# Performance work log

Measured on AMD Instinct MI355X. Metric: run time of the kernel, lower is better.

The kernel has to match this reference:

```python
import jax, jax.numpy as jnp
import numpy as np

BN_EPS = 1e-5

def conv3x3(x, w, b):
    # x: (B,C,H,W), w: (O,C,3,3) -> (B,O,H,W), padding=1 == SAME for 3x3 stride 1
    y = jax.lax.conv_general_dilated(x, w, window_strides=(1, 1), padding='SAME',
                                     dimension_numbers=('NCHW', 'OIHW', 'NCHW'))
    return y + b[None, :, None, None]

def batchnorm(x, gamma, beta):
    # training-mode BatchNorm2d: per-channel batch stats over (N,H,W), biased variance
    mean = jnp.mean(x, axis=(0, 2, 3), keepdims=True)
    var = jnp.var(x, axis=(0, 2, 3), keepdims=True)
    return (x - mean) * jax.lax.rsqrt(var + BN_EPS) * gamma[None, :, None, None] + beta[None, :, None, None]


def setup_inputs() -> dict:
    key = jax.random.key(0)
    ks = jax.random.split(key, 4)
    B, E, T, Fr, H = 16, 16, 1024, 80, 8
    # xavier-ish scale for conv weights
    w_in = jax.random.normal(ks[1], (3 * H, E, 3, 3), jnp.float32) * (1.0 / np.sqrt(E * 9))
    w_out = jax.random.normal(ks[2], (E, 2 * H, 3, 3), jnp.float32) * (1.0 / np.sqrt(2 * H * 9))
    return {
        'x': jax.random.normal(ks[0], (B, E, T, Fr), jnp.float32),
        'w_in': w_in,
        'b_in': jnp.zeros((3 * H,), jnp.float32),
        'w_out': w_out,
        'b_out': jnp.zeros((E,), jnp.float32),
        'gq': jnp.ones((H,), jnp.float32), 'bq': jnp.zeros((H,), jnp.float32),
        'gk': jnp.ones((H,), jnp.float32), 'bk': jnp.zeros((H,), jnp.float32),
        'gv': jnp.ones((H,), jnp.float32), 'bv': jnp.zeros((H,), jnp.float32),
        'go': jnp.ones((E,), jnp.float32), 'bo': jnp.zeros((E,), jnp.float32),
    }


def reference(x, w_in, b_in, w_out, b_out, gq, bq, gk, bk, gv, bv, go, bo):
    B, E, T, Fr = x.shape
    H = w_in.shape[0] // 3
    scaling = E ** (-0.5)  # head_dim == embed_dim in this module

    qkv = conv3x3(x, w_in, b_in)                      # (B, 3H, T, F)
    q, k, v = jnp.split(qkv, 3, axis=1)               # each (B, H, T, F)
    q = q * scaling

    q = jax.nn.relu(batchnorm(q, gq, bq)).reshape(B * H, T, Fr)
    k = jax.nn.relu(batchnorm(k, gk, bk)).reshape(B * H, T, Fr)
    v = jax.nn.relu(batchnorm(v, gv, bv)).reshape(B * H, T, Fr)

    # time-axis attention: (BH,T,F) x (BH,S,F) -> (BH,T,S)
    aw_t = jax.nn.softmax(jnp.einsum('btf,bsf->bts', q, k), axis=-1)
    attn_t = jnp.einsum('bts,bsf->btf', aw_t, v)      # (BH, T, F)

    # freq-axis attention: q^T @ k -> (BH,F,F); then @ v^T -> (BH,F,T)
    aw_f = jax.nn.softmax(jnp.einsum('btf,btg->bfg', q, k), axis=-1)
    attn_f = jnp.einsum('bfg,btg->bft', aw_f, v)      # (BH, F, T)

    attn_t = attn_t.reshape(B, H, T, Fr)
    attn_f = attn_f.transpose(0, 2, 1).reshape(B, H, T, Fr)
    attn = jnp.concatenate([attn_t, attn_f], axis=1)  # (B, 2H, T, F)

    out = jax.nn.relu(batchnorm(conv3x3(attn, w_out, b_out), go, bo))  # (B, E, T, F)
    aw_t_avg = aw_t.reshape(B, H, T, T).sum(axis=1) / H                # (B, T, T)
    return out, aw_t_avg
```

## Files before the change

kernel.cpp:

```cpp
#include <hip/hip_runtime.h>
#include <cstdint>
#include <cstddef>

#define NB 16
#define NT 1024
#define NF 80
#define NH 8
#define FP 96
#define FS 84
#define SP 1032
#define KP 108
#define VP 264

typedef _Float16 v8h __attribute__((ext_vector_type(8)));
typedef _Float16 v4h __attribute__((ext_vector_type(4)));
typedef _Float16 v2h __attribute__((ext_vector_type(2)));
typedef float v4f __attribute__((ext_vector_type(4)));

static const size_t OUT_ELEMS = (size_t)NB * 16 * NT * NF;

__global__ __launch_bounds__(256) void cl_k(const float* __restrict__ src,
                                            _Float16* __restrict__ dst) {
  const int b = blockIdx.y, t0 = blockIdx.x * 16;
  for (int i = threadIdx.x; i < 16 * FS; i += 256) {
    int lt = i / FS, s = i % FS;
    int t = t0 + lt, f = s - 1;
    v8h lo = (v8h)(_Float16)0.f, hi = (v8h)(_Float16)0.f;
    if (f >= 0 && f < NF) {
#pragma unroll
      for (int c = 0; c < 8; ++c)
        lo[c] = (_Float16)src[((size_t)(b * 16 + c) * NT + t) * NF + f];
#pragma unroll
      for (int c = 0; c < 8; ++c)
        hi[c] = (_Float16)src[((size_t)(b * 16 + 8 + c) * NT + t) * NF + f];
    }
    _Float16* d = dst + ((size_t)(b * NT + t) * FS + s) * 16;
    *(v8h*)d = lo;
    *(v8h*)(d + 8) = hi;
  }
}

template <int OCT, int OSTRIDE, bool QSCALE, bool PADOUT>
__global__ __launch_bounds__(512) void conv_mfma_k(
    const _Float16* __restrict__ xcl, const float* __restrict__ w,
    const float* __restrict__ bias, _Float16* __restrict__ out, int CO) {
  __shared__ _Float16 axt[18][FS * 16];
  __shared__ _Float16 wlds[3][2][OCT * 16][32];
  __shared__ float blds[32];
  const int b = blockIdx.y, t0 = blockIdx.x * 16;
  const int tid = threadIdx.x;
  const int NW = 3 * 2 * OCT * 16 * 32;
  for (int i = tid; i < NW; i += 512) {
    int kk = i % 32;
    int oc = (i / 32) % (OCT * 16);
    int ck = (i / (32 * OCT * 16)) % 2;
    int kt = i / (64 * OCT * 16);
    int kg = ck * 32 + kk;
    float v = 0.f;
    if (oc < CO && kg < 48) {
      int c = kg & 15, kf = kg >> 4;
      v = w[((oc * 16 + c) * 3 + kt) * 3 + kf];
      if (QSCALE && oc < 8) v *= 0.25f;
    }
    wlds[kt][ck][oc][kk] = (_Float16)v;
  }
  if (tid < 32) {
    float v = (tid < CO) ? bias[tid] : 0.f;
    if (QSCALE && tid < 8) v *= 0.25f;
    blds[tid] = v;
  }
  for (int i = tid; i < 18 * 168; i += 512) {
    int r = i / 168, j = i % 168;
    int t = t0 + r - 1;
    int4 v = {0, 0, 0, 0};
    if (t >= 0 && t < NT)
      v = ((const int4*)(xcl + (size_t)(b * NT + t) * FS * 16))[j];
    ((int4*)axt[r])[j] = v;
  }
  __syncthreads();
  const int wv = tid >> 6, l = tid & 63, lg = l >> 4, lm = l & 15;
  v8h bfr[3][2][OCT];
#pragma unroll
  for (int kt = 0; kt < 3; ++kt)
#pragma unroll
    for (int ck = 0; ck < 2; ++ck)
#pragma unroll
      for (int ot = 0; ot < OCT; ++ot)
        bfr[kt][ck][ot] = *(const v8h*)&wlds[kt][ck][ot * 16 + lm][lg * 8];
#pragma unroll
  for (int li = 0; li < 2; ++li) {
    const int lt = wv * 2 + li;
    const int tt = t0 + lt;
#pragma unroll
    for (int f0 = 0; f0 < 80; f0 += 16) {
      v4f acc[OCT];
#pragma unroll
      for (int ot = 0; ot < OCT; ++ot) acc[ot] = (v4f){0.f, 0.f, 0.f, 0.f};
#pragma unroll
      for (int kt = 0; kt < 3; ++kt)
#pragma unroll
        for (int ck = 0; ck < 2; ++ck) {
          v8h afr =
              *(const v8h*)&axt[lt + kt][(f0 + lm) * 16 + ck * 32 + lg * 8];
#pragma unroll
          for (int ot = 0; ot < OCT; ++ot)
            acc[ot] = __builtin_amdgcn_mfma_f32_16x16x32_f16(
                afr, bfr[kt][ck][ot], acc[ot], 0, 0, 0);
        }
#pragma unroll
      for (int ot = 0; ot < OCT; ++ot) {
        int oc = ot * 16 + lm;
        if (oc < CO) {
          float bv = blds[oc];
          v4h o;
#pragma unroll
          for (int r = 0; r < 4; ++r) o[r] = (_Float16)(acc[ot][r] + bv);
          *(v4h*)(out + ((size_t)(b * CO + oc) * NT + tt) * OSTRIDE + f0 +
                  lg * 4) = o;
        }
      }
    }
  }
  if constexpr (PADOUT) {
    for (int i = tid; i < CO * 16 * 2; i += 512) {
      int oc = i / 32, lt2 = (i / 2) % 16, half = i & 1;
      int4 z = {0, 0, 0, 0};
      ((int4*)(out + ((size_t)(b * CO + oc) * NT + t0 + lt2) * OSTRIDE +
               80))[half] = z;
    }
  }
}

__global__ __launch_bounds__(256) void bn_stats_h_k(
    const _Float16* __restrict__ x, float* __restrict__ partials) {
  const int b = blockIdx.x, c = blockIdx.y;
  const v8h* p = (const v8h*)(x + (size_t)(b * 24 + c) * NT * FP);
  float s = 0.f, s2 = 0.f;
  for (int i = threadIdx.x; i < NT * FP / 8; i += 256) {
    v8h v = p[i];
#pragma unroll
    for (int j = 0; j < 8; ++j) {
      float f = (float)v[j];
      s += f;
      s2 += f * f;
    }
  }
  __shared__ float rs[256], rs2[256];
  rs[threadIdx.x] = s;
  rs2[threadIdx.x] = s2;
  __syncthreads();
  for (int off = 128; off > 0; off >>= 1) {
    if ((int)threadIdx.x < off) {
      rs[threadIdx.x] += rs[threadIdx.x + off];
      rs2[threadIdx.x] += rs2[threadIdx.x + off];
    }
    __syncthreads();
  }
  if (threadIdx.x == 0) {
    partials[(c * 16 + b) * 2 + 0] = rs[0];
    partials[(c * 16 + b) * 2 + 1] = rs2[0];
  }
}

__global__ __launch_bounds__(256) void bn_stats_y_k(
    const _Float16* __restrict__ x, float* __restrict__ partials) {
  const int b = blockIdx.x, c = blockIdx.y;
  const v8h* p = (const v8h*)(x + (size_t)(b * 16 + c) * (NT * NF));
  float s = 0.f, s2 = 0.f;
  for (int i = threadIdx.x; i < NT * NF / 8; i += 256) {
    v8h v = p[i];
#pragma unroll
    for (int j = 0; j < 8; ++j) {
      float f = (float)v[j];
      s += f;
      s2 += f * f;
    }
  }
  __shared__ float rs[256], rs2[256];
  rs[threadIdx.x] = s;
  rs2[threadIdx.x] = s2;
  __syncthreads();
  for (int off = 128; off > 0; off >>= 1) {
    if ((int)threadIdx.x < off) {
      rs[threadIdx.x] += rs[threadIdx.x + off];
      rs2[threadIdx.x] += rs2[threadIdx.x + off];
    }
    __syncthreads();
  }
  if (threadIdx.x == 0) {
    partials[(c * 16 + b) * 2 + 0] = rs[0];
    partials[(c * 16 + b) * 2 + 1] = rs2[0];
  }
}

__global__ void bn_finalize_k(const float* __restrict__ partials,
                              float* __restrict__ stats, int C) {
  int c = threadIdx.x;
  if (c < C) {
    float s = 0.f, s2 = 0.f;
    for (int i = 0; i < 16; ++i) {
      s += partials[(c * 16 + i) * 2 + 0];
      s2 += partials[(c * 16 + i) * 2 + 1];
    }
    const float N = 16.0f * (float)(NT * NF);
    float mean = s / N;
    float var = s2 / N - mean * mean;
    stats[c * 2 + 0] = mean;
    stats[c * 2 + 1] = rsqrtf(var + 1e-5f);
  }
}

__global__ __launch_bounds__(256) void bn_apply_qkv_k(
    _Float16* __restrict__ qkv, const float* __restrict__ stats,
    const float* __restrict__ gq, const float* __restrict__ bq,
    const float* __restrict__ gk, const float* __restrict__ bk,
    const float* __restrict__ gv, const float* __restrict__ bv) {
  const size_t n8 = (size_t)NB * 24 * NT * 12;
  const size_t stride = (size_t)gridDim.x * blockDim.x;
  for (size_t idx = (size_t)blockIdx.x * blockDim.x + threadIdx.x; idx < n8;
       idx += stride) {
    int fc = (int)(idx % 12);
    if (fc >= 10) continue;
    int c = (int)((idx / (NT * 12)) % 24);
    float g, be;
    if (c < 8) { g = gq[c]; be = bq[c]; }
    else if (c < 16) { g = gk[c - 8]; be = bk[c - 8]; }
    else { g = gv[c - 16]; be = bv[c - 16]; }
    float mean = stats[c * 2 + 0], invstd = stats[c * 2 + 1];
    v8h v = ((v8h*)qkv)[idx];
#pragma unroll
    for (int j = 0; j < 8; ++j) {
      float f = (float)v[j];
      f = fmaxf((f - mean) * invstd * g + be, 0.f);
      v[j] = (_Float16)f;
    }
    ((v8h*)qkv)[idx] = v;
  }
}

__global__ __launch_bounds__(256) void vtrans_k(
    const _Float16* __restrict__ qkv, _Float16* __restrict__ vT) {
  __shared__ _Float16 tile[128 * 100];
  const int tc = blockIdx.x, bh = blockIdx.y;
  const int b = bh >> 3, h = bh & 7;
  const int t0 = tc * 128;
  const _Float16* src = qkv + ((size_t)(b * 24 + 16 + h) * NT + t0) * FP;
  const int tid = threadIdx.x;
  for (int i = tid; i < 1536; i += 256) {
    int row = i / 12, c = i % 12;
    int4 v = ((const int4*)src)[i];
    int2* d = (int2*)&tile[row * 100 + c * 8];
    d[0] = make_int2(v.x, v.y);
    d[1] = make_int2(v.z, v.w);
  }
  __syncthreads();
  _Float16* dst = vT + (size_t)bh * 80 * NT + t0;
  for (int i = tid; i < 1280; i += 256) {
    int f = i / 16, c8 = i % 16;
    v8h v;
#pragma unroll
    for (int j = 0; j < 8; ++j) v[j] = tile[(c8 * 8 + j) * 100 + f];
    *(v8h*)(dst + (size_t)f * NT + c8 * 8) = v;
  }
}

__global__ __launch_bounds__(512) void time_attn_k(
    const _Float16* __restrict__ qkv, const _Float16* __restrict__ vT,
    float* __restrict__ attn_out, float* __restrict__ aw_avg) {
  __shared__ _Float16 s_lds[32 * SP];
  __shared__ _Float16 q_lds[32 * KP];
  __shared__ _Float16 kst[256 * KP];
  __shared__ float inv_lds[32];
  const int b = blockIdx.y, t0 = blockIdx.x * 32;
  const int tid = threadIdx.x;
  const int w = tid >> 6, l = tid & 63, lg = l >> 4, lm = l & 15;
  const int grp = tid >> 5, lane = tid & 31;
  float avg[2][32];
#pragma unroll
  for (int rr = 0; rr < 2; ++rr)
#pragma unroll
    for (int k = 0; k < 32; ++k) avg[rr][k] = 0.f;

  int4 rb[6];
  auto gloadK = [&](const _Float16* base, int chunk) {
    const int4* src = (const int4*)(base + (size_t)chunk * 256 * FP);
#pragma unroll
    for (int u = 0; u < 6; ++u) rb[u] = src[tid + u * 512];
  };
  auto lwriteK = [&]() {
#pragma unroll
    for (int u = 0; u < 6; ++u) {
      int i = tid + u * 512, row = i / 12, j = i % 12;
      int2* d = (int2*)&kst[row * KP + j * 8];
      d[0] = make_int2(rb[u].x, rb[u].y);
      d[1] = make_int2(rb[u].z, rb[u].w);
    }
  };
  auto gloadV = [&](const int4* vt4, int chunk) {
#pragma unroll
    for (int u = 0; u < 5; ++u) {
      int i = tid + u * 512, row = i >> 5, c = i & 31;
      rb[u] = vt4[row * 128 + chunk * 32 + c];
    }
  };
  auto lwriteV = [&]() {
#pragma unroll
    for (int u = 0; u < 5; ++u) {
      int i = tid + u * 512, row = i >> 5, c = i & 31;
      *(int4*)&kst[row * VP + c * 8] = rb[u];
    }
  };

  gloadK(qkv + (size_t)(b * 24 + 8) * NT * FP, 0);

  for (int h = 0; h < NH; ++h) {
    const _Float16* qb = qkv + ((size_t)(b * 24 + h) * NT + t0) * FP;
    const _Float16* kb = qkv + (size_t)(b * 24 + 8 + h) * NT * FP;
    const int4* vt4 = (const int4*)(vT + (size_t)(b * 8 + h) * 80 * NT);
    int4 qreg = {0, 0, 0, 0};
    if (tid < 384) qreg = ((const int4*)qb)[tid];
    lwriteK();
    if (tid < 384) {
      int row = tid / 12, j = tid % 12;
      int2* d = (int2*)&q_lds[row * KP + j * 8];
      d[0] = make_int2(qreg.x, qreg.y);
      d[1] = make_int2(qreg.z, qreg.w);
    }
    gloadK(kb, 1);
    __syncthreads();
    v8h afr[2][3];
#pragma unroll
    for (int qt = 0; qt < 2; ++qt)
#pragma unroll
      for (int kk = 0; kk < 3; ++kk) {
        v4h a0 = *(const v4h*)&q_lds[(qt * 16 + lm) * KP + kk * 32 + lg * 8];
        v4h a1 =
            *(const v4h*)&q_lds[(qt * 16 + lm) * KP + kk * 32 + lg * 8 + 4];
        afr[qt][kk] = __builtin_shufflevector(a0, a1, 0, 1, 2, 3, 4, 5, 6, 7);
      }
    v4f accO[2][5];
#pragma unroll
    for (int qt = 0; qt < 2; ++qt)
#pragma unroll
      for (int ft = 0; ft < 5; ++ft) accO[qt][ft] = (v4f){0.f, 0.f, 0.f, 0.f};

    for (int s = 0; s < 8; ++s) {
      if (s == 4) {
#pragma unroll
        for (int rr = 0; rr < 2; ++rr) {
          const int row = grp + rr * 16;
          _Float16* srow = &s_lds[row * SP];
          float m = -1e30f;
#pragma unroll
          for (int k = 0; k < 16; ++k) {
            v2h e2 = *(const v2h*)&srow[lane * 2 + k * 64];
            m = fmaxf(m, fmaxf((float)e2[0], (float)e2[1]));
          }
#pragma unroll
          for (int mk = 16; mk; mk >>= 1) m = fmaxf(m, __shfl_xor(m, mk, 32));
          float d = 0.f;
#pragma unroll
          for (int k = 0; k < 16; ++k) {
            v2h e2 = *(const v2h*)&srow[lane * 2 + k * 64];
            float e0 = __expf((float)e2[0] - m);
            float e1 = __expf((float)e2[1] - m);
            d += e0 + e1;
            v2h w2;
            w2[0] = (_Float16)e0;
            w2[1] = (_Float16)e1;
            *(v2h*)&srow[lane * 2 + k * 64] = w2;
          }
#pragma unroll
          for (int mk = 16; mk; mk >>= 1) d += __shfl_xor(d, mk, 32);
          float inv = 1.f / d;
          if (lane == 0) inv_lds[row] = inv;
#pragma unroll
          for (int k = 0; k < 16; ++k) {
            v2h e2 = *(const v2h*)&srow[lane * 2 + k * 64];
            avg[rr][2 * k] += (float)e2[0] * inv;
            avg[rr][2 * k + 1] += (float)e2[1] * inv;
          }
        }
        __syncthreads();
      }
      if (s < 4) {
#pragma unroll
        for (int tt = 0; tt < 2; ++tt) {
          const int rowb = (w * 2 + tt) * 16;
          const int rbase = (rowb + lm) * KP;
          v8h bfr[3];
#pragma unroll
          for (int kk = 0; kk < 3; ++kk) {
            v4h b0 = *(const v4h*)&kst[rbase + kk * 32 + lg * 8];
            v4h b1 = *(const v4h*)&kst[rbase + kk * 32 + lg * 8 + 4];
            bfr[kk] = __builtin_shufflevector(b0, b1, 0, 1, 2, 3, 4, 5, 6, 7);
          }
          const int sc = s * 256 + rowb + lm;
#pragma unroll
          for (int qt = 0; qt < 2; ++qt) {
            v4f acc = (v4f){0.f, 0.f, 0.f, 0.f};
#pragma unroll
            for (int kk = 0; kk < 3; ++kk)
              acc = __builtin_amdgcn_mfma_f32_16x16x32_f16(afr[qt][kk],
                                                           bfr[kk], acc, 0, 0,
                                                           0);
#pragma unroll
            for (int r = 0; r < 4; ++r)
              s_lds[(qt * 16 + lg * 4 + r) * SP + sc] = (_Float16)acc[r];
          }
        }
      } else {
        const int vcb = (s - 4) * 256;
        v8h pfr[2];
#pragma unroll
        for (int qt = 0; qt < 2; ++qt)
          pfr[qt] =
              *(const v8h*)&s_lds[(qt * 16 + lm) * SP + vcb + w * 32 + lg * 8];
#pragma unroll
        for (int ft = 0; ft < 5; ++ft) {
          v8h bfr = *(const v8h*)&kst[(ft * 16 + lm) * VP + w * 32 + lg * 8];
          accO[0][ft] = __builtin_amdgcn_mfma_f32_16x16x32_f16(
              pfr[0], bfr, accO[0][ft], 0, 0, 0);
          accO[1][ft] = __builtin_amdgcn_mfma_f32_16x16x32_f16(
              pfr[1], bfr, accO[1][ft], 0, 0, 0);
        }
      }
      __syncthreads();
      if (s < 7) {
        if (s + 1 < 4) lwriteK(); else lwriteV();
        int ns = s + 2;
        if (ns < 4) gloadK(kb, ns);
        else if (ns < 8) gloadV(vt4, ns - 4);
        else if (h < 7)
          gloadK(qkv + (size_t)(b * 24 + 8 + h + 1) * NT * FP, 0);
        __syncthreads();
      }
    }
    float* ored = (float*)s_lds;
#pragma unroll
    for (int qt = 0; qt < 2; ++qt) {
#pragma unroll
      for (int ft = 0; ft < 5; ++ft)
#pragma unroll
        for (int r = 0; r < 4; ++r)
          ored[(w * 16 + lg * 4 + r) * 84 + ft * 16 + lm] =
              accO[qt][ft][r] * inv_lds[qt * 16 + lg * 4 + r];
      __syncthreads();
      for (int i = tid; i < 1280; i += 512) {
        int q = i / 80, f = i % 80;
        float ss = 0.f;
#pragma unroll
        for (int ww = 0; ww < 8; ++ww) ss += ored[(ww * 16 + q) * 84 + f];
        attn_out[((size_t)(b * 16 + h) * NT + t0 + qt * 16 + q) * NF + f] = ss;
      }
      __syncthreads();
    }
  }
#pragma unroll
  for (int rr = 0; rr < 2; ++rr) {
    float* ab = aw_avg + ((size_t)b * NT + t0 + grp + rr * 16) * NT;
#pragma unroll
    for (int k = 0; k < 16; ++k) {
      float2 v2;
      v2.x = avg[rr][2 * k] * 0.125f;
      v2.y = avg[rr][2 * k + 1] * 0.125f;
      *(float2*)&ab[lane * 2 + k * 64] = v2;
    }
  }
}

__global__ __launch_bounds__(64) void freq_qk_k(
    const _Float16* __restrict__ qkv, float* __restrict__ Cp) {
  __shared__ _Float16 qs[128 * 100];
  __shared__ _Float16 ks[128 * 100];
  const int tc = blockIdx.x, bh = blockIdx.y;
  const int b = bh >> 3, h = bh & 7;
  const int t0 = tc * 128;
  const _Float16* qb = qkv + ((size_t)(b * 24 + h) * NT + t0) * FP;
  const _Float16* kb = qkv + ((size_t)(b * 24 + 8 + h) * NT + t0) * FP;
  const int tid = threadIdx.x;
  for (int i = tid; i < 1536; i += 64) {
    int row = i / 12, c = i % 12;
    int4 vq = ((const int4*)qb)[i];
    int4 vk = ((const int4*)kb)[i];
    int2* dq = (int2*)&qs[row * 100 + c * 8];
    dq[0] = make_int2(vq.x, vq.y);
    dq[1] = make_int2(vq.z, vq.w);
    int2* dk = (int2*)&ks[row * 100 + c * 8];
    dk[0] = make_int2(vk.x, vk.y);
    dk[1] = make_int2(vk.z, vk.w);
  }
  __syncthreads();
  const int lg = tid >> 4, lm = tid & 15;
  v4f acc[5][5];
#pragma unroll
  for (int fr = 0; fr < 5; ++fr)
#pragma unroll
    for (int gc = 0; gc < 5; ++gc) acc[fr][gc] = (v4f){0.f, 0.f, 0.f, 0.f};
#pragma unroll
  for (int kk = 0; kk < 4; ++kk) {
    v8h afr[5];
#pragma unroll
    for (int fr = 0; fr < 5; ++fr)
#pragma unroll
      for (int j = 0; j < 8; ++j)
        afr[fr][j] = qs[(kk * 32 + lg * 8 + j) * 100 + fr * 16 + lm];
#pragma unroll
    for (int gc = 0; gc < 5; ++gc) {
      v8h bfr;
#pragma unroll
      for (int j = 0; j < 8; ++j)
        bfr[j] = ks[(kk * 32 + lg * 8 + j) * 100 + gc * 16 + lm];
#pragma unroll
      for (int fr = 0; fr < 5; ++fr)
        acc[fr][gc] = __builtin_amdgcn_mfma_f32_16x16x32_f16(afr[fr], bfr,
                                                             acc[fr][gc], 0,
                                                             0, 0);
    }
  }
  float* cpb = Cp + ((size_t)bh * 8 + tc) * 6400;
#pragma unroll
  for (int fr = 0; fr < 5; ++fr)
#pragma unroll
    for (int gc = 0; gc < 5; ++gc)
#pragma unroll
      for (int r = 0; r < 4; ++r)
        cpb[(fr * 16 + lg * 4 + r) * 80 + gc * 16 + lm] = acc[fr][gc][r];
}

__global__ __launch_bounds__(128) void freq_sm_k(const float* __restrict__ Cp,
                                                 _Float16* __restrict__ P) {
  const int bh = blockIdx.x;
  const int f = threadIdx.x;
  if (f >= 80) return;
  float c[80];
#pragma unroll
  for (int g = 0; g < 80; ++g) c[g] = 0.f;
  const float* base = Cp + (size_t)bh * 8 * 6400 + f * 80;
#pragma unroll
  for (int tc = 0; tc < 8; ++tc) {
    const float4* p4 = (const float4*)(base + tc * 6400);
#pragma unroll
    for (int g4 = 0; g4 < 20; ++g4) {
      float4 v = p4[g4];
      c[g4 * 4 + 0] += v.x;
      c[g4 * 4 + 1] += v.y;
      c[g4 * 4 + 2] += v.z;
      c[g4 * 4 + 3] += v.w;
    }
  }
  float m = -1e30f;
#pragma unroll
  for (int g = 0; g < 80; ++g) m = fmaxf(m, c[g]);
  float d = 0.f;
#pragma unroll
  for (int g = 0; g < 80; ++g) {
    float e = __expf(c[g] - m);
    d += e;
    c[g] = e;
  }
  float inv = 1.f / d;
  _Float16* pb = P + (size_t)bh * 80 * 96 + (size_t)f * 96;
#pragma unroll
  for (int c8 = 0; c8 < 10; ++c8) {
    v8h v;
#pragma unroll
    for (int j = 0; j < 8; ++j) v[j] = (_Float16)(c[c8 * 8 + j] * inv);
    *(v8h*)(pb + c8 * 8) = v;
  }
  v8h z = (v8h)(_Float16)0.f;
  *(v8h*)(pb + 80) = z;
  *(v8h*)(pb + 88) = z;
}

__global__ __launch_bounds__(256) void freq_pv_k(
    const _Float16* __restrict__ qkv, const _Float16* __restrict__ P,
    float* __restrict__ attn_out) {
  __shared__ _Float16 vs[128 * 104];
  __shared__ _Float16 ps[80 * 104];
  const int tc = blockIdx.x, bh = blockIdx.y;
  const int b = bh >> 3, h = bh & 7;
  const int t0 = tc * 128;
  const _Float16* vb = qkv + ((size_t)(b * 24 + 16 + h) * NT + t0) * FP;
  const _Float16* pb = P + (size_t)bh * 80 * 96;
  const int tid = threadIdx.x;
  for (int i = tid; i < 1536; i += 256) {
    int row = i / 12, c = i % 12;
    *(int4*)&vs[row * 104 + c * 8] = ((const int4*)vb)[i];
  }
  for (int i = tid; i < 960; i += 256) {
    int row = i / 12, c = i % 12;
    *(int4*)&ps[row * 104 + c * 8] = ((const int4*)pb)[i];
  }
  __syncthreads();
  const int w = tid >> 6, l = tid & 63, lg = l >> 4, lm = l & 15;
  v8h bfr[5][3];
#pragma unroll
  for (int fc = 0; fc < 5; ++fc)
#pragma unroll
    for (int kk = 0; kk < 3; ++kk)
      bfr[fc][kk] = *(const v8h*)&ps[(fc * 16 + lm) * 104 + kk * 32 + lg * 8];
#pragma unroll
  for (int tt2 = 0; tt2 < 2; ++tt2) {
    const int tt = w + tt2 * 4;
    v8h afr[3];
#pragma unroll
    for (int kk = 0; kk < 3; ++kk)
      afr[kk] = *(const v8h*)&vs[(tt * 16 + lm) * 104 + kk * 32 + lg * 8];
    float* ob =
        attn_out + ((size_t)(b * 16 + 8 + h) * NT + t0 + tt * 16) * NF;
#pragma unroll
    for (int fc = 0; fc < 5; ++fc) {
      v4f acc = (v4f){0.f, 0.f, 0.f, 0.f};
#pragma unroll
      for (int kk = 0; kk < 3; ++kk)
        acc = __builtin_amdgcn_mfma_f32_16x16x32_f16(afr[kk], bfr[fc][kk],
                                                     acc, 0, 0, 0);
#pragma unroll
      for (int r = 0; r < 4; ++r)
        ob[(lg * 4 + r) * NF + fc * 16 + lm] = acc[r];
    }
  }
}

__global__ __launch_bounds__(256) void bn_apply_out_k(
    const _Float16* __restrict__ y, const float* __restrict__ stats,
    const float* __restrict__ go, const float* __restrict__ bo,
    float* __restrict__ out) {
  const size_t n8 = OUT_ELEMS / 8;
  const size_t stride = (size_t)gridDim.x * blockDim.x;
  for (size_t idx = (size_t)blockIdx.x * blockDim.x + threadIdx.x; idx < n8;
       idx += stride) {
    int c = (int)((idx / (NT * NF / 8)) % 16);
    float g = go[c], be = bo[c];
    float mean = stats[c * 2 + 0], invstd = stats[c * 2 + 1];
    v8h v = ((const v8h*)y)[idx];
    float4 o0, o1;
    o0.x = fmaxf(((float)v[0] - mean) * invstd * g + be, 0.f);
    o0.y = fmaxf(((float)v[1] - mean) * invstd * g + be, 0.f);
    o0.z = fmaxf(((float)v[2] - mean) * invstd * g + be, 0.f);
    o0.w = fmaxf(((float)v[3] - mean) * invstd * g + be, 0.f);
    o1.x = fmaxf(((float)v[4] - mean) * invstd * g + be, 0.f);
    o1.y = fmaxf(((float)v[5] - mean) * invstd * g + be, 0.f);
    o1.z = fmaxf(((float)v[6] - mean) * invstd * g + be, 0.f);
    o1.w = fmaxf(((float)v[7] - mean) * invstd * g + be, 0.f);
    ((float4*)out)[idx * 2] = o0;
    ((float4*)out)[idx * 2 + 1] = o1;
  }
}

extern "C" void kernel_launch(void* const* d_in, const int* in_sizes, int n_in,
                              void* d_out, int out_size, void* d_ws,
                              size_t ws_size, hipStream_t stream) {
  const float* x = (const float*)d_in[0];
  const float* w_in = (const float*)d_in[1];
  const float* b_in = (const float*)d_in[2];
  const float* w_out = (const float*)d_in[3];
  const float* b_out = (const float*)d_in[4];
  const float* gq = (const float*)d_in[5];
  const float* bq = (const float*)d_in[6];
  const float* gk = (const float*)d_in[7];
  const float* bk = (const float*)d_in[8];
  const float* gv = (const float*)d_in[9];
  const float* bv = (const float*)d_in[10];
  const float* go = (const float*)d_in[11];
  const float* bo = (const float*)d_in[12];

  float* out = (float*)d_out;
  float* aw = out + OUT_ELEMS;
  char* wsb = (char*)d_ws;
  _Float16* qkvb = (_Float16*)wsb;
  _Float16* yh = (_Float16*)wsb;
  _Float16* xcl = (_Float16*)(wsb + 75497472);
  _Float16* acl = xcl;
  _Float16* vTb = (_Float16*)(wsb + 75497472);
  float* Cp = (float*)(wsb + 75497472);
  _Float16* Pf = (_Float16*)(wsb + 101711872);
  float* partials = (float*)(wsb + 119537664);
  float* stats1 = partials + 768;
  float* stats2 = stats1 + 48;

  cl_k<<<dim3(64, 16), 256, 0, stream>>>(x, xcl);
  conv_mfma_k<2, FP, true, true>
      <<<dim3(64, 16), 512, 0, stream>>>(xcl, w_in, b_in, qkvb, 24);
  bn_stats_h_k<<<dim3(16, 24), 256, 0, stream>>>(qkvb, partials);
  bn_finalize_k<<<1, 64, 0, stream>>>(partials, stats1, 24);
  bn_apply_qkv_k<<<2048, 256, 0, stream>>>(qkvb, stats1, gq, bq, gk, bk, gv,
                                           bv);
  vtrans_k<<<dim3(8, 128), 256, 0, stream>>>(qkvb, vTb);
  time_attn_k<<<dim3(32, 16), 512, 0, stream>>>(qkvb, vTb, out, aw);
  freq_qk_k<<<dim3(8, 128), 64, 0, stream>>>(qkvb, Cp);
  freq_sm_k<<<128, 128, 0, stream>>>(Cp, Pf);
  freq_pv_k<<<dim3(8, 128), 256, 0, stream>>>(qkvb, Pf, out);
  cl_k<<<dim3(64, 16), 256, 0, stream>>>(out, acl);
  conv_mfma_k<1, NF, false, false>
      <<<dim3(64, 16), 512, 0, stream>>>(acl, w_out, b_out, yh, 16);
  bn_stats_y_k<<<dim3(16, 16), 256, 0, stream>>>(yh, partials);
  bn_finalize_k<<<1, 64, 0, stream>>>(partials, stats2, 16);
  bn_apply_out_k<<<2048, 256, 0, stream>>>(yh, stats2, go, bo, out);
}
```

Before: 455.3 us.

## Fuse BN statistics into conv epilogue and widen time attention to 1024 threads

The conv kernels now accumulate per-channel sum and sum-of-squares of their fp32 outputs, reduce them across the wave and block, and write per-block partials. A new finalize kernel reduces these partials. This removes the separate passes that re-read the fp16 qkv and output tensors just for statistics. Separately, time_attn_k moves from 512 to 1024 threads per block: each wave handles one key tile and the PV work is split across two frequency halves, trading higher register pressure for more parallelism per block. Statistics are now taken from fp32 values before the fp16 cast, so they differ slightly.

```diff
diff --git a/kernel.cpp b/kernel.cpp
--- a/kernel.cpp
+++ b/kernel.cpp
@@ -43,10 +43,12 @@
 template <int OCT, int OSTRIDE, bool QSCALE, bool PADOUT>
 __global__ __launch_bounds__(512) void conv_mfma_k(
     const _Float16* __restrict__ xcl, const float* __restrict__ w,
-    const float* __restrict__ bias, _Float16* __restrict__ out, int CO) {
+    const float* __restrict__ bias, _Float16* __restrict__ out,
+    float* __restrict__ pstats, int CO) {
   __shared__ _Float16 axt[18][FS * 16];
   __shared__ _Float16 wlds[3][2][OCT * 16][32];
   __shared__ float blds[32];
+  __shared__ float wsum[8][OCT][16], wsq[8][OCT][16];
   const int b = blockIdx.y, t0 = blockIdx.x * 16;
   const int tid = threadIdx.x;
   const int NW = 3 * 2 * OCT * 16 * 32;
@@ -87,6 +89,9 @@
 #pragma unroll
       for (int ot = 0; ot < OCT; ++ot)
         bfr[kt][ck][ot] = *(const v8h*)&wlds[kt][ck][ot * 16 + lm][lg * 8];
+  float s1[OCT], s2[OCT];
+#pragma unroll
+  for (int ot = 0; ot < OCT; ++ot) { s1[ot] = 0.f; s2[ot] = 0.f; }
 #pragma unroll
   for (int li = 0; li < 2; ++li) {
     const int lt = wv * 2 + li;
@@ -114,7 +119,12 @@
           float bv = blds[oc];
           v4h o;
 #pragma unroll
-          for (int r = 0; r < 4; ++r) o[r] = (_Float16)(acc[ot][r] + bv);
+          for (int r = 0; r < 4; ++r) {
+            float v = acc[ot][r] + bv;
+            s1[ot] += v;
+            s2[ot] += v * v;
+            o[r] = (_Float16)v;
+          }
           *(v4h*)(out + ((size_t)(b * CO + oc) * NT + tt) * OSTRIDE + f0 +
                   lg * 4) = o;
         }
@@ -129,25 +139,38 @@
                80))[half] = z;
     }
   }
-}
-
-__global__ __launch_bounds__(256) void bn_stats_h_k(
-    const _Float16* __restrict__ x, float* __restrict__ partials) {
-  const int b = blockIdx.x, c = blockIdx.y;
-  const v8h* p = (const v8h*)(x + (size_t)(b * 24 + c) * NT * FP);
-  float s = 0.f, s2 = 0.f;
-  for (int i = threadIdx.x; i < NT * FP / 8; i += 256) {
-    v8h v = p[i];
-#pragma unroll
-    for (int j = 0; j < 8; ++j) {
-      float f = (float)v[j];
-      s += f;
-      s2 += f * f;
-    }
+#pragma unroll
+  for (int ot = 0; ot < OCT; ++ot) {
+    float a = s1[ot], b2 = s2[ot];
+    a += __shfl_xor(a, 16);
+    a += __shfl_xor(a, 32);
+    b2 += __shfl_xor(b2, 16);
+    b2 += __shfl_xor(b2, 32);
+    if (l < 16) { wsum[wv][ot][lm] = a; wsq[wv][ot][lm] = b2; }
+  }
+  __syncthreads();
+  if (tid < CO) {
+    int ot = tid >> 4, lmm = tid & 15;
+    float a = 0.f, b2 = 0.f;
+#pragma unroll
+    for (int w2 = 0; w2 < 8; ++w2) { a += wsum[w2][ot][lmm]; b2 += wsq[w2][ot][lmm]; }
+    int bid = blockIdx.y * 64 + blockIdx.x;
+    pstats[tid * 1024 + bid] = a;
+    pstats[(CO + tid) * 1024 + bid] = b2;
+  }
+}
+
+__global__ __launch_bounds__(256) void bn_finalize2_k(
+    const float* __restrict__ pstats, float* __restrict__ stats, int C) {
+  const int c = blockIdx.x;
+  float a = 0.f, b2 = 0.f;
+  for (int i = threadIdx.x; i < 1024; i += 256) {
+    a += pstats[c * 1024 + i];
+    b2 += pstats[(C + c) * 1024 + i];
   }
   __shared__ float rs[256], rs2[256];
-  rs[threadIdx.x] = s;
-  rs2[threadIdx.x] = s2;
+  rs[threadIdx.x] = a;
+  rs2[threadIdx.x] = b2;
   __syncthreads();
   for (int off = 128; off > 0; off >>= 1) {
     if ((int)threadIdx.x < off) {
@@ -157,54 +180,9 @@
     __syncthreads();
   }
   if (threadIdx.x == 0) {
-    partials[(c * 16 + b) * 2 + 0] = rs[0];
-    partials[(c * 16 + b) * 2 + 1] = rs2[0];
-  }
-}
-
-__global__ __launch_bounds__(256) void bn_stats_y_k(
-    const _Float16* __restrict__ x, float* __restrict__ partials) {
-  const int b = blockIdx.x, c = blockIdx.y;
-  const v8h* p = (const v8h*)(x + (size_t)(b * 16 + c) * (NT * NF));
-  float s = 0.f, s2 = 0.f;
-  for (int i = threadIdx.x; i < NT * NF / 8; i += 256) {
-    v8h v = p[i];
-#pragma unroll
-    for (int j = 0; j < 8; ++j) {
-      float f = (float)v[j];
-      s += f;
-      s2 += f * f;
-    }
-  }
-  __shared__ float rs[256], rs2[256];
-  rs[threadIdx.x] = s;
-  rs2[threadIdx.x] = s2;
-  __syncthreads();
-  for (int off = 128; off > 0; off >>= 1) {
-    if ((int)threadIdx.x < off) {
-      rs[threadIdx.x] += rs[threadIdx.x + off];
-      rs2[threadIdx.x] += rs2[threadIdx.x + off];
-    }
-    __syncthreads();
-  }
-  if (threadIdx.x == 0) {
-    partials[(c * 16 + b) * 2 + 0] = rs[0];
-    partials[(c * 16 + b) * 2 + 1] = rs2[0];
-  }
-}
-
-__global__ void bn_finalize_k(const float* __restrict__ partials,
-                              float* __restrict__ stats, int C) {
-  int c = threadIdx.x;
-  if (c < C) {
-    float s = 0.f, s2 = 0.f;
-    for (int i = 0; i < 16; ++i) {
-      s += partials[(c * 16 + i) * 2 + 0];
-      s2 += partials[(c * 16 + i) * 2 + 1];
-    }
     const float N = 16.0f * (float)(NT * NF);
-    float mean = s / N;
-    float var = s2 / N - mean * mean;
+    float mean = rs[0] / N;
+    float var = rs2[0] / N - mean * mean;
     stats[c * 2 + 0] = mean;
     stats[c * 2 + 1] = rsqrtf(var + 1e-5f);
   }
@@ -264,7 +242,7 @@
   }
 }
 
-__global__ __launch_bounds__(512) void time_attn_k(
+__global__ __launch_bounds__(1024) void time_attn_k(
     const _Float16* __restrict__ qkv, const _Float16* __restrict__ vT,
     float* __restrict__ attn_out, float* __restrict__ aw_avg) {
   __shared__ _Float16 s_lds[32 * SP];
@@ -275,22 +253,21 @@
   const int tid = threadIdx.x;
   const int w = tid >> 6, l = tid & 63, lg = l >> 4, lm = l & 15;
   const int grp = tid >> 5, lane = tid & 31;
-  float avg[2][32];
-#pragma unroll
-  for (int rr = 0; rr < 2; ++rr)
-#pragma unroll
-    for (int k = 0; k < 32; ++k) avg[rr][k] = 0.f;
-
-  int4 rb[6];
+  const int ks = w >> 1, fh = w & 1;
+  float avg[32];
+#pragma unroll
+  for (int k = 0; k < 32; ++k) avg[k] = 0.f;
+
+  int4 rb[3];
   auto gloadK = [&](const _Float16* base, int chunk) {
     const int4* src = (const int4*)(base + (size_t)chunk * 256 * FP);
 #pragma unroll
-    for (int u = 0; u < 6; ++u) rb[u] = src[tid + u * 512];
+    for (int u = 0; u < 3; ++u) rb[u] = src[tid + u * 1024];
   };
   auto lwriteK = [&]() {
 #pragma unroll
-    for (int u = 0; u < 6; ++u) {
-      int i = tid + u * 512, row = i / 12, j = i % 12;
+    for (int u = 0; u < 3; ++u) {
+      int i = tid + u * 1024, row = i / 12, j = i % 12;
       int2* d = (int2*)&kst[row * KP + j * 8];
       d[0] = make_int2(rb[u].x, rb[u].y);
       d[1] = make_int2(rb[u].z, rb[u].w);
@@ -298,16 +275,22 @@
   };
   auto gloadV = [&](const int4* vt4, int chunk) {
 #pragma unroll
-    for (int u = 0; u < 5; ++u) {
-      int i = tid + u * 512, row = i >> 5, c = i & 31;
-      rb[u] = vt4[row * 128 + chunk * 32 + c];
+    for (int u = 0; u < 3; ++u) {
+      int i = tid + u * 1024;
+      if (i < 2560) {
+        int row = i >> 5, c = i & 31;
+        rb[u] = vt4[row * 128 + chunk * 32 + c];
+      }
     }
   };
   auto lwriteV = [&]() {
 #pragma unroll
-    for (int u = 0; u < 5; ++u) {
-      int i = tid + u * 512, row = i >> 5, c = i & 31;
-      *(int4*)&kst[row * VP + c * 8] = rb[u];
+    for (int u = 0; u < 3; ++u) {
+      int i = tid + u * 1024;
+      if (i < 2560) {
+        int row = i >> 5, c = i & 31;
+        *(int4*)&kst[row * VP + c * 8] = rb[u];
+      }
     }
   };
 
@@ -338,91 +321,86 @@
             *(const v4h*)&q_lds[(qt * 16 + lm) * KP + kk * 32 + lg * 8 + 4];
         afr[qt][kk] = __builtin_shufflevector(a0, a1, 0, 1, 2, 3, 4, 5, 6, 7);
       }
-    v4f accO[2][5];
+    v4f accO[2][3];
 #pragma unroll
     for (int qt = 0; qt < 2; ++qt)
 #pragma unroll
-      for (int ft = 0; ft < 5; ++ft) accO[qt][ft] = (v4f){0.f, 0.f, 0.f, 0.f};
+      for (int fi = 0; fi < 3; ++fi) accO[qt][fi] = (v4f){0.f, 0.f, 0.f, 0.f};
 
     for (int s = 0; s < 8; ++s) {
       if (s == 4) {
-#pragma unroll
-        for (int rr = 0; rr < 2; ++rr) {
-          const int row = grp + rr * 16;
-          _Float16* srow = &s_lds[row * SP];
-          float m = -1e30f;
-#pragma unroll
-          for (int k = 0; k < 16; ++k) {
-            v2h e2 = *(const v2h*)&srow[lane * 2 + k * 64];
-            m = fmaxf(m, fmaxf((float)e2[0], (float)e2[1]));
-          }
-#pragma unroll
-          for (int mk = 16; mk; mk >>= 1) m = fmaxf(m, __shfl_xor(m, mk, 32));
-          float d = 0.f;
-#pragma unroll
-          for (int k = 0; k < 16; ++k) {
-            v2h e2 = *(const v2h*)&srow[lane * 2 + k * 64];
-            float e0 = __expf((float)e2[0] - m);
-            float e1 = __expf((float)e2[1] - m);
-            d += e0 + e1;
-            v2h w2;
-            w2[0] = (_Float16)e0;
-            w2[1] = (_Float16)e1;
-            *(v2h*)&srow[lane * 2 + k * 64] = w2;
-          }
-#pragma unroll
-          for (int mk = 16; mk; mk >>= 1) d += __shfl_xor(d, mk, 32);
-          float inv = 1.f / d;
-          if (lane == 0) inv_lds[row] = inv;
-#pragma unroll
-          for (int k = 0; k < 16; ++k) {
-            v2h e2 = *(const v2h*)&srow[lane * 2 + k * 64];
-            avg[rr][2 * k] += (float)e2[0] * inv;
-            avg[rr][2 * k + 1] += (float)e2[1] * inv;
-          }
+        _Float16* srow = &s_lds[grp * SP];
+        float m = -1e30f;
+#pragma unroll
+        for (int k = 0; k < 16; ++k) {
+          v2h e2 = *(const v2h*)&srow[lane * 2 + k * 64];
+          m = fmaxf(m, fmaxf((float)e2[0], (float)e2[1]));
+        }
+#pragma unroll
+        for (int mk = 16; mk; mk >>= 1) m = fmaxf(m, __shfl_xor(m, mk, 32));
+        float d = 0.f;
+#pragma unroll
+        for (int k = 0; k < 16; ++k) {
+          v2h e2 = *(const v2h*)&srow[lane * 2 + k * 64];
+          float e0 = __expf((float)e2[0] - m);
+          float e1 = __expf((float)e2[1] - m);
+          d += e0 + e1;
+          v2h w2;
+          w2[0] = (_Float16)e0;
+          w2[1] = (_Float16)e1;
+          *(v2h*)&srow[lane * 2 + k * 64] = w2;
+        }
+#pragma unroll
+        for (int mk = 16; mk; mk >>= 1) d += __shfl_xor(d, mk, 32);
+        float inv = 1.f / d;
+        if (lane == 0) inv_lds[grp] = inv;
+#pragma unroll
+        for (int k = 0; k < 16; ++k) {
+          v2h e2 = *(const v2h*)&srow[lane * 2 + k * 64];
+          avg[2 * k] += (float)e2[0] * inv;
+          avg[2 * k + 1] += (float)e2[1] * inv;
         }
         __syncthreads();
       }
       if (s < 4) {
-#pragma unroll
-        for (int tt = 0; tt < 2; ++tt) {
-          const int rowb = (w * 2 + tt) * 16;
-          const int rbase = (rowb + lm) * KP;
-          v8h bfr[3];
-#pragma unroll
-          for (int kk = 0; kk < 3; ++kk) {
-            v4h b0 = *(const v4h*)&kst[rbase + kk * 32 + lg * 8];
-            v4h b1 = *(const v4h*)&kst[rbase + kk * 32 + lg * 8 + 4];
-            bfr[kk] = __builtin_shufflevector(b0, b1, 0, 1, 2, 3, 4, 5, 6, 7);
-          }
-          const int sc = s * 256 + rowb + lm;
-#pragma unroll
-          for (int qt = 0; qt < 2; ++qt) {
-            v4f acc = (v4f){0.f, 0.f, 0.f, 0.f};
-#pragma unroll
-            for (int kk = 0; kk < 3; ++kk)
-              acc = __builtin_amdgcn_mfma_f32_16x16x32_f16(afr[qt][kk],
-                                                           bfr[kk], acc, 0, 0,
-                                                           0);
-#pragma unroll
-            for (int r = 0; r < 4; ++r)
-              s_lds[(qt * 16 + lg * 4 + r) * SP + sc] = (_Float16)acc[r];
-          }
+        const int rbase = (w * 16 + lm) * KP;
+        v8h bfr[3];
+#pragma unroll
+        for (int kk = 0; kk < 3; ++kk) {
+          v4h b0 = *(const v4h*)&kst[rbase + kk * 32 + lg * 8];
+          v4h b1 = *(const v4h*)&kst[rbase + kk * 32 + lg * 8 + 4];
+          bfr[kk] = __builtin_shufflevector(b0, b1, 0, 1, 2, 3, 4, 5, 6, 7);
+        }
+        const int sc = s * 256 + w * 16 + lm;
+#pragma unroll
+        for (int qt = 0; qt < 2; ++qt) {
+          v4f acc = (v4f){0.f, 0.f, 0.f, 0.f};
+#pragma unroll
+          for (int kk = 0; kk < 3; ++kk)
+            acc = __builtin_amdgcn_mfma_f32_16x16x32_f16(afr[qt][kk], bfr[kk],
+                                                         acc, 0, 0, 0);
+#pragma unroll
+          for (int r = 0; r < 4; ++r)
+            s_lds[(qt * 16 + lg * 4 + r) * SP + sc] = (_Float16)acc[r];
         }
       } else {
         const int vcb = (s - 4) * 256;
         v8h pfr[2];
 #pragma unroll
         for (int qt = 0; qt < 2; ++qt)
-          pfr[qt] =
-              *(const v8h*)&s_lds[(qt * 16 + lm) * SP + vcb + w * 32 + lg * 8];
-#pragma unroll
-        for (int ft = 0; ft < 5; ++ft) {
-          v8h bfr = *(const v8h*)&kst[(ft * 16 + lm) * VP + w * 32 + lg * 8];
-          accO[0][ft] = __builtin_amdgcn_mfma_f32_16x16x32_f16(
-              pfr[0], bfr, accO[0][ft], 0, 0, 0);
-          accO[1][ft] = __builtin_amdgcn_mfma_f32_16x16x32_f16(
-              pfr[1], bfr, accO[1][ft], 0, 0, 0);
+          pfr[qt] = *(const v8h*)&s_lds[(qt * 16 + lm) * SP + vcb + ks * 32 +
+                                        lg * 8];
+#pragma unroll
+        for (int fi = 0; fi < 3; ++fi) {
+          int ft = fh * 3 + fi;
+          if (ft < 5) {
+            v8h bfr =
+                *(const v8h*)&kst[(ft * 16 + lm) * VP + ks * 32 + lg * 8];
+            accO[0][fi] = __builtin_amdgcn_mfma_f32_16x16x32_f16(
+                pfr[0], bfr, accO[0][fi], 0, 0, 0);
+            accO[1][fi] = __builtin_amdgcn_mfma_f32_16x16x32_f16(
+                pfr[1], bfr, accO[1][fi], 0, 0, 0);
+          }
         }
       }
       __syncthreads();
@@ -440,13 +418,17 @@
 #pragma unroll
     for (int qt = 0; qt < 2; ++qt) {
 #pragma unroll
-      for (int ft = 0; ft < 5; ++ft)
-#pragma unroll
-        for (int r = 0; r < 4; ++r)
-          ored[(w * 16 + lg * 4 + r) * 84 + ft * 16 + lm] =
-              accO[qt][ft][r] * inv_lds[qt * 16 + lg * 4 + r];
+      for (int fi = 0; fi < 3; ++fi) {
+        int ft = fh * 3 + fi;
+        if (ft < 5) {
+#pragma unroll
+          for (int r = 0; r < 4; ++r)
+            ored[(ks * 16 + lg * 4 + r) * 84 + ft * 16 + lm] =
+                accO[qt][fi][r] * inv_lds[qt * 16 + lg * 4 + r];
+        }
+      }
       __syncthreads();
-      for (int i = tid; i < 1280; i += 512) {
+      for (int i = tid; i < 1280; i += 1024) {
         int q = i / 80, f = i % 80;
         float ss = 0.f;
 #pragma unroll
@@ -456,14 +438,13 @@
       __syncthreads();
     }
   }
-#pragma unroll
-  for (int rr = 0; rr < 2; ++rr) {
-    float* ab = aw_avg + ((size_t)b * NT + t0 + grp + rr * 16) * NT;
+  {
+    float* ab = aw_avg + ((size_t)b * NT + t0 + grp) * NT;
 #pragma unroll
     for (int k = 0; k < 16; ++k) {
       float2 v2;
-      v2.x = avg[rr][2 * k] * 0.125f;
-      v2.y = avg[rr][2 * k + 1] * 0.125f;
+      v2.x = avg[2 * k] * 0.125f;
+      v2.y = avg[2 * k + 1] * 0.125f;
       *(float2*)&ab[lane * 2 + k * 64] = v2;
     }
   }
@@ -676,26 +657,24 @@
   _Float16* vTb = (_Float16*)(wsb + 75497472);
   float* Cp = (float*)(wsb + 75497472);
   _Float16* Pf = (_Float16*)(wsb + 101711872);
-  float* partials = (float*)(wsb + 119537664);
-  float* stats1 = partials + 768;
+  float* pstats = (float*)(wsb + 119537664);
+  float* stats1 = pstats + 49152;
   float* stats2 = stats1 + 48;
 
   cl_k<<<dim3(64, 16), 256, 0, stream>>>(x, xcl);
   conv_mfma_k<2, FP, true, true>
-      <<<dim3(64, 16), 512, 0, stream>>>(xcl, w_in, b_in, qkvb, 24);
-  bn_stats_h_k<<<dim3(16, 24), 256, 0, stream>>>(qkvb, partials);
-  bn_finalize_k<<<1, 64, 0, stream>>>(partials, stats1, 24);
+      <<<dim3(64, 16), 512, 0, stream>>>(xcl, w_in, b_in, qkvb, pstats, 24);
+  bn_finalize2_k<<<24, 256, 0, stream>>>(pstats, stats1, 24);
   bn_apply_qkv_k<<<2048, 256, 0, stream>>>(qkvb, stats1, gq, bq, gk, bk, gv,
                                            bv);
   vtrans_k<<<dim3(8, 128), 256, 0, stream>>>(qkvb, vTb);
-  time_attn_k<<<dim3(32, 16), 512, 0, stream>>>(qkvb, vTb, out, aw);
+  time_attn_k<<<dim3(32, 16), 1024, 0, stream>>>(qkvb, vTb, out, aw);
   freq_qk_k<<<dim3(8, 128), 64, 0, stream>>>(qkvb, Cp);
   freq_sm_k<<<128, 128, 0, stream>>>(Cp, Pf);
   freq_pv_k<<<dim3(8, 128), 256, 0, stream>>>(qkvb, Pf, out);
   cl_k<<<dim3(64, 16), 256, 0, stream>>>(out, acl);
   conv_mfma_k<1, NF, false, false>
-      <<<dim3(64, 16), 512, 0, stream>>>(acl, w_out, b_out, yh, 16);
-  bn_stats_y_k<<<dim3(16, 16), 256, 0, stream>>>(yh, partials);
-  bn_finalize_k<<<1, 64, 0, stream>>>(partials, stats2, 16);
+      <<<dim3(64, 16), 512, 0, stream>>>(acl, w_out, b_out, yh, pstats, 16);
+  bn_finalize2_k<<<16, 256, 0, stream>>>(pstats, stats2, 16);
   bn_apply_out_k<<<2048, 256, 0, stream>>>(yh, stats2, go, bo, out);
 }
```

After: 482.5 us. +6.0%, slower.
